# Optimization experiments

Measured on AMD Instinct MI355X. Metric: run time of the kernel, lower is better.

## Reference

```python
import jax, jax.numpy as jnp
import numpy as np

B, C, T = 8, 512, 2048
INTER = C // 2            # inter_channels default = in_channels // 2
L = 2                     # temporal_layer_num


def _pos_encoding(c, t):
    # standard sinusoidal PE, returned as (c, t) to match pos().permute(0,2,1)
    pos = jnp.arange(t, dtype=jnp.float32)[:, None]            # (t,1)
    i = jnp.arange(0, c, 2, dtype=jnp.float32)                 # (c/2,)
    div = jnp.exp(-(jnp.log(10000.0) / c) * i)                 # (c/2,)
    pe = jnp.zeros((t, c), dtype=jnp.float32)
    pe = pe.at[:, 0::2].set(jnp.sin(pos * div))
    pe = pe.at[:, 1::2].set(jnp.cos(pos * div))
    return pe.T                                                # (c,t)


def _conv1x1(w, b, x):
    # kernel_size=1 Conv1d == channel GEMM: w (o,c), x (b,c,t) -> (b,o,t)
    return jnp.einsum('oc,bct->bot', w, x) + b[:, None]


def _temporal_conv(x, w, d):
    # Conv2d(1, c, kernel=(3, c), dilation=(d,1), padding=(d,0), no bias)
    # x (b,c,t) -> input (b,1,t,c); kernel w (c,3,c) -> (c,1,3,c); out (b,c,t,1)
    x4 = x.transpose(0, 2, 1)[:, None, :, :]
    k = w[:, None, :, :]
    y = jax.lax.conv_general_dilated(
        x4, k, window_strides=(1, 1), padding=((d, d), (0, 0)),
        rhs_dilation=(d, 1), dimension_numbers=('NCHW', 'OIHW', 'NCHW'))
    return y[..., 0]                                           # (b,c,t)


def setup_inputs() -> dict:
    key = jax.random.key(0)
    ks = jax.random.split(key, 12)
    n = lambda k, shape, s=0.02: jax.random.normal(k, shape, jnp.float32) * s
    return {
        'x': jax.random.normal(ks[0], (B, C, T), jnp.float32),
        'w_tr': n(ks[1], (C, C)),
        'b_tr': jnp.zeros((C,), jnp.float32),
        'w_tc': n(ks[2], (L, C, 3, C), 0.001),   # init.normal_(std=0.001)
        'w_g': n(ks[3], (L + 1, INTER, C)),
        'b_g': jnp.zeros((L + 1, INTER), jnp.float32),
        'w_th': n(ks[4], (L + 1, INTER, C)),
        'b_th': jnp.zeros((L + 1, INTER), jnp.float32),
        'w_ph': n(ks[5], (L + 1, INTER, C)),
        'b_ph': jnp.zeros((L + 1, INTER), jnp.float32),
        'w_W': n(ks[6], (C, INTER * (L + 1))),
        'b_W': jnp.zeros((C,), jnp.float32),
        'gamma': 1.0 + n(ks[7], (C,)),
        'beta': n(ks[8], (C,)),
    }


def reference(x, w_tr, b_tr, w_tc, w_g, b_g, w_th, b_th, w_ph, b_ph,
              w_W, b_W, gamma, beta):
    b, c, t = x.shape
    x = x + _pos_encoding(c, t)[None]                 # add positional encoding
    x = jax.nn.relu(_conv1x1(w_tr, b_tr, x))          # tranpos_w + relu

    # temporal dilated-conv features, then raw x as last branch
    temps = [_temporal_conv(x, w_tc[i], i + 1) for i in range(w_tc.shape[0])]
    temps.append(x)

    ys = []
    for i, tx in enumerate(temps):
        gx = _conv1x1(w_g[i], b_g[i], tx)             # (b,inter,t)
        th = _conv1x1(w_th[i], b_th[i], tx)           # (b,inter,t)
        ph = _conv1x1(w_ph[i], b_ph[i], tx)           # (b,inter,t)
        f = jax.nn.softmax(jnp.einsum('bit,bis->bts', th, ph), axis=-1)
        ys.append(jnp.einsum('bts,bis->bit', f, gx))  # (b,inter,t)

    y = jnp.concatenate(ys, axis=1)                   # (b, 3*inter, t)
    wy = _conv1x1(w_W, b_W, y)                        # (b,c,t)
    # BatchNorm1d, training-mode batch stats over (batch, time)
    mean = wy.mean(axis=(0, 2), keepdims=True)
    var = wy.var(axis=(0, 2), keepdims=True)
    wy = (wy - mean) * jax.lax.rsqrt(var + 1e-5)
    wy = wy * gamma[None, :, None] + beta[None, :, None]
    return wy + x
```

## Files before the change

kernel.cpp:

```cpp
#include <hip/hip_runtime.h>

#define B_ 8
#define C_ 512
#define T_ 2048
#define I_ 256
#define TP_ (T_ + 4)

typedef _Float16 f16x8 __attribute__((ext_vector_type(8)));
typedef float f32x4 __attribute__((ext_vector_type(4)));
typedef unsigned short u16;
typedef unsigned short u16x4 __attribute__((ext_vector_type(4)));

__device__ __forceinline__ u16 f2h(float f) {
    _Float16 h = (_Float16)f;
    return *(u16*)&h;
}
__device__ __forceinline__ float h2f(u16 u) {
    _Float16 h = *(_Float16*)&u;
    return (float)h;
}

#define AS1 __attribute__((address_space(1)))
#define AS3 __attribute__((address_space(3)))
__device__ __forceinline__ void gload16(const u16* g, u16* l) {
    __builtin_amdgcn_global_load_lds((const AS1 void*)(const void*)g,
                                     (AS3 void*)(void*)l, 16, 0, 0);
}

template <int WMODE, bool BIAS, bool RELU, bool TCONV>
__global__ __launch_bounds__(256) void mfma_gemm(
    const u16* __restrict__ A, long aB, int aZdiv, int lda,
    const u16* __restrict__ Bm, long bB, int ldb, int bZmod,
    const float* __restrict__ bias, int biasStride,
    float* __restrict__ Cf, u16* __restrict__ Cn, long cB, int ldc,
    u16* __restrict__ Ct, long ctB, int ldct, int ctOff,
    int K, int dShift)
{
    __shared__ u16 sA[128 * 64];
    __shared__ u16 sB[128 * 64];
    const int z = blockIdx.z;
    const int zw = z / aZdiv;
    const int zb = z % bZmod;
    const int m0 = blockIdx.y * 128, n0 = blockIdx.x * 128;
    const int tid = threadIdx.x;
    const int lane = tid & 63, wv = tid >> 6;
    const int wm = wv >> 1, wn = wv & 1;
    const int l15 = lane & 15, l4 = lane >> 4;

    const u16* Ab = A + (long)zw * aB + (long)m0 * lda;
    const u16* Bb = Bm + (long)zb * bB + (long)n0 * ldb;

    const int srow = wv * 32 + (lane >> 3);
    const int sk16 = (lane & 7) ^ (lane >> 3);

    f32x4 acc[4][4];
    #pragma unroll
    for (int i = 0; i < 4; ++i)
        #pragma unroll
        for (int j = 0; j < 4; ++j) acc[i][j] = (f32x4){0.f, 0.f, 0.f, 0.f};

    for (int k0 = 0; k0 < K; k0 += 64) {
        int bCol = k0;
        int rOff = 0;
        if (TCONV) {
            const int kh = k0 >> 9;
            const int d = dShift ? dShift : 1 + (z >> 3);
            rOff = (kh - 1) * d;
            bCol = k0 & 511;
        }
        #pragma unroll
        for (int ch = 0; ch < 4; ++ch) {
            gload16(Ab + (long)(srow + ch * 8) * lda + k0 + sk16 * 8,
                    &sA[wv * 2048 + ch * 512]);
            gload16(Bb + (long)(srow + ch * 8 + rOff) * ldb + bCol + sk16 * 8,
                    &sB[wv * 2048 + ch * 512]);
        }
        __syncthreads();
        #pragma unroll
        for (int kk = 0; kk < 2; ++kk) {
            f16x8 af[4], bfr[4];
            #pragma unroll
            for (int f = 0; f < 4; ++f) {
                const int ra = wm * 64 + f * 16 + l15;
                af[f] = *(const f16x8*)&sA[ra * 64 + ((((kk << 2) | l4) ^ (ra & 7)) << 3)];
                const int rb = wn * 64 + f * 16 + l15;
                bfr[f] = *(const f16x8*)&sB[rb * 64 + ((((kk << 2) | l4) ^ (rb & 7)) << 3)];
            }
            #pragma unroll
            for (int mi = 0; mi < 4; ++mi)
                #pragma unroll
                for (int ni = 0; ni < 4; ++ni)
                    acc[mi][ni] = __builtin_amdgcn_mfma_f32_16x16x32_f16(
                        af[mi], bfr[ni], acc[mi][ni], 0, 0, 0);
        }
        __syncthreads();
    }

    #pragma unroll
    for (int mi = 0; mi < 4; ++mi) {
        const int mb = m0 + wm * 64 + mi * 16 + l4 * 4;
        float bv[4] = {0.f, 0.f, 0.f, 0.f};
        if (BIAS) {
            const float* bp = bias + (long)zw * biasStride;
            #pragma unroll
            for (int r = 0; r < 4; ++r) bv[r] = bp[mb + r];
        }
        #pragma unroll
        for (int ni = 0; ni < 4; ++ni) {
            const int nb = n0 + wn * 64 + ni * 16 + l15;
            float v[4];
            #pragma unroll
            for (int r = 0; r < 4; ++r) {
                v[r] = acc[mi][ni][r] + bv[r];
                if (RELU) v[r] = fmaxf(v[r], 0.f);
            }
            if (WMODE & 1) {
                #pragma unroll
                for (int r = 0; r < 4; ++r)
                    Cf[(long)z * cB + (long)(mb + r) * ldc + nb] = v[r];
            }
            if (WMODE & 2) {
                #pragma unroll
                for (int r = 0; r < 4; ++r)
                    Cn[(long)z * cB + (long)(mb + r) * ldc + nb] = f2h(v[r]);
            }
            if (WMODE & 4) {
                u16x4 pk;
                #pragma unroll
                for (int r = 0; r < 4; ++r) pk[r] = f2h(v[r]);
                *(u16x4*)&Ct[(long)z * ctB + (long)nb * ldct + ctOff + mb] = pk;
            }
        }
    }
}

__global__ __launch_bounds__(512) void flash_attn(
    const u16* __restrict__ thA, const u16* __restrict__ phA,
    const u16* __restrict__ gxA, u16* __restrict__ oH,
    float* __restrict__ mH, float* __restrict__ lH)
{
    __shared__ u16 sK[64 * 256];
    __shared__ u16 sV[256 * 64];
    __shared__ u16 sP[8 * 16 * 64];

    const int flat = (blockIdx.z * 24 + blockIdx.y) * 16 + blockIdx.x;
    const int swz = (flat & 7) * 96 + (flat >> 3);
    const int u = swz % 384;
    const int qb = u & 15, z = u >> 4;
    const int half = swz / 384;
    const int t0 = qb * 128;
    const int sBase = half * (T_ / 2);
    const int tid = threadIdx.x;
    const int lane = tid & 63, wv = tid >> 6;
    const int l15 = lane & 15, l4 = lane >> 4;

    const u16* Qz = thA + (long)z * (T_ * I_);
    const u16* Kz = phA + (long)z * (T_ * I_);
    const u16* Vz = gxA + (long)z * ((long)I_ * T_);

    f16x8 qf[8];
    {
        const u16* qrow = Qz + (long)(t0 + wv * 16 + l15) * I_ + l4 * 8;
        #pragma unroll
        for (int ks = 0; ks < 8; ++ks) qf[ks] = *(const f16x8*)(qrow + ks * 32);
    }

    f32x4 oacc[16];
    #pragma unroll
    for (int i = 0; i < 16; ++i) oacc[i] = (f32x4){0.f, 0.f, 0.f, 0.f};
    float mrun[4] = {-1e30f, -1e30f, -1e30f, -1e30f};
    float lrun[4] = {0.f, 0.f, 0.f, 0.f};

    const int krow = tid >> 5;
    const int kk16 = (tid & 31) ^ (krow & 7);
    const int vrow = tid >> 3;
    const int vk16 = (tid & 7) ^ (vrow & 7);

    for (int s0 = sBase; s0 < sBase + T_ / 2; s0 += 64) {
        #pragma unroll
        for (int is = 0; is < 4; ++is) {
            gload16(Kz + (long)(s0 + is * 16 + krow) * I_ + kk16 * 8,
                    &sK[is * 4096 + tid * 8]);
            gload16(Vz + (long)(is * 64 + vrow) * T_ + s0 + vk16 * 8,
                    &sV[is * 4096 + tid * 8]);
        }
        __syncthreads();

        f32x4 sacc[4];
        #pragma unroll
        for (int nf = 0; nf < 4; ++nf) sacc[nf] = (f32x4){0.f, 0.f, 0.f, 0.f};
        #pragma unroll
        for (int nf = 0; nf < 4; ++nf) {
            const int srow = nf * 16 + l15;
            #pragma unroll
            for (int ks = 0; ks < 8; ++ks) {
                f16x8 kf = *(const f16x8*)&sK[srow * 256 + ((((ks << 2) | l4) ^ (srow & 7)) << 3)];
                sacc[nf] = __builtin_amdgcn_mfma_f32_16x16x32_f16(qf[ks], kf, sacc[nf], 0, 0, 0);
            }
        }

        float scale[4];
        #pragma unroll
        for (int r = 0; r < 4; ++r) {
            float v0 = fmaxf(fmaxf(sacc[0][r], sacc[1][r]),
                             fmaxf(sacc[2][r], sacc[3][r]));
            #pragma unroll
            for (int o = 8; o; o >>= 1) v0 = fmaxf(v0, __shfl_xor(v0, o, 64));
            const float mnew = fmaxf(mrun[r], v0);
            scale[r] = __expf(mrun[r] - mnew);
            mrun[r] = mnew;
        }
        float rsum[4] = {0.f, 0.f, 0.f, 0.f};
        #pragma unroll
        for (int nf = 0; nf < 4; ++nf) {
            #pragma unroll
            for (int r = 0; r < 4; ++r) {
                const float p = __expf(sacc[nf][r] - mrun[r]);
                rsum[r] += p;
                const int tl = l4 * 4 + r;
                const int sl = l15 + nf * 16;
                sP[wv * 1024 + tl * 64 + ((((sl >> 3) ^ (tl & 7)) << 3) | (sl & 7))] = f2h(p);
            }
        }
        #pragma unroll
        for (int r = 0; r < 4; ++r) {
            #pragma unroll
            for (int o = 8; o; o >>= 1) rsum[r] += __shfl_xor(rsum[r], o, 64);
            lrun[r] = lrun[r] * scale[r] + rsum[r];
        }
        #pragma unroll
        for (int nf = 0; nf < 16; ++nf)
            #pragma unroll
            for (int r = 0; r < 4; ++r) oacc[nf][r] *= scale[r];

        f16x8 pa[2];
        #pragma unroll
        for (int kk = 0; kk < 2; ++kk)
            pa[kk] = *(const f16x8*)&sP[wv * 1024 + l15 * 64 + ((((kk << 2) | l4) ^ (l15 & 7)) << 3)];
        #pragma unroll
        for (int nf = 0; nf < 16; ++nf) {
            const int dvr = nf * 16 + l15;
            #pragma unroll
            for (int kk = 0; kk < 2; ++kk) {
                f16x8 vf = *(const f16x8*)&sV[dvr * 64 + ((((kk << 2) | l4) ^ (dvr & 7)) << 3)];
                oacc[nf] = __builtin_amdgcn_mfma_f32_16x16x32_f16(pa[kk], vf, oacc[nf], 0, 0, 0);
            }
        }
        __syncthreads();
    }

    #pragma unroll
    for (int r = 0; r < 4; ++r) {
        const int t = t0 + wv * 16 + l4 * 4 + r;
        const long row = ((long)half * 24 + z) * T_ + t;
        u16* dst = oH + row * I_ + l15;
        #pragma unroll
        for (int nf = 0; nf < 16; ++nf)
            dst[nf * 16] = f2h(oacc[nf][r]);
        if (l15 == 0) { mH[row] = mrun[r]; lH[row] = lrun[r]; }
    }
}

__global__ __launch_bounds__(256) void combine_kernel(
    const u16* __restrict__ oH, const float* __restrict__ mH,
    const float* __restrict__ lH, u16* __restrict__ YT)
{
    const long idx = (long)blockIdx.x * 256 + threadIdx.x;
    const int z = (int)(idx / (T_ * (I_ / 8)));
    const long rem = idx % (T_ * (I_ / 8));
    const int t = (int)(rem / (I_ / 8));
    const int dv0 = (int)(rem % (I_ / 8)) * 8;
    const long row0 = (long)z * T_ + t;
    const long row1 = ((long)24 + z) * T_ + t;
    const float m0 = mH[row0], m1 = mH[row1];
    const float l0 = lH[row0], l1 = lH[row1];
    const float m = fmaxf(m0, m1);
    const float a0 = __expf(m0 - m), a1 = __expf(m1 - m);
    const float inv = 1.f / (l0 * a0 + l1 * a1);
    const uint4 p0 = *(const uint4*)&oH[row0 * I_ + dv0];
    const uint4 p1 = *(const uint4*)&oH[row1 * I_ + dv0];
    const u16* b0 = (const u16*)&p0;
    const u16* b1 = (const u16*)&p1;
    uint4 ov;
    u16* bo = (u16*)&ov;
    #pragma unroll
    for (int j = 0; j < 8; ++j)
        bo[j] = f2h((h2f(b0[j]) * a0 + h2f(b1[j]) * a1) * inv);
    const int br = z >> 3, b = z & 7;
    *(uint4*)&YT[((long)b * T_ + t) * (3 * I_) + br * I_ + dv0] = ov;
}

__global__ __launch_bounds__(256) void to_f16(
    const float* __restrict__ s, u16* __restrict__ d, long n4)
{
    const long i = (long)blockIdx.x * 256 + threadIdx.x;
    if (i >= n4) return;
    const float4 v = ((const float4*)s)[i];
    u16x4 pk = {f2h(v.x), f2h(v.y), f2h(v.z), f2h(v.w)};
    ((u16x4*)d)[i] = pk;
}

__global__ __launch_bounds__(256) void peT_kernel(float* __restrict__ peT)
{
    const int idx = blockIdx.x * 256 + threadIdx.x;
    const int c = idx & (C_ - 1), t = idx >> 9;
    const float i2 = (float)(c & ~1);
    const float freq = expf(-(9.210340371976184f / (float)C_) * i2);
    const float ang = (float)t * freq;
    peT[idx] = (c & 1) ? cosf(ang) : sinf(ang);
}

__global__ __launch_bounds__(256) void xpose_add(
    const float* __restrict__ x, const float* __restrict__ peT,
    u16* __restrict__ xpeT)
{
    __shared__ float tile[64][65];
    const int b = blockIdx.z;
    const int t0 = blockIdx.x * 64, c0 = blockIdx.y * 64;
    const int rr = threadIdx.x >> 4, cc4 = (threadIdx.x & 15) << 2;
    #pragma unroll
    for (int p = 0; p < 4; ++p) {
        const int row = rr + p * 16;
        const float4 v = *(const float4*)&x[((long)b * C_ + c0 + row) * T_ + t0 + cc4];
        tile[row][cc4 + 0] = v.x; tile[row][cc4 + 1] = v.y;
        tile[row][cc4 + 2] = v.z; tile[row][cc4 + 3] = v.w;
    }
    __syncthreads();
    #pragma unroll
    for (int p = 0; p < 4; ++p) {
        const int tt = rr + p * 16;
        const int gt = t0 + tt;
        const float4 pv = *(const float4*)&peT[(long)gt * C_ + c0 + cc4];
        u16x4 pk = {f2h(tile[cc4 + 0][tt] + pv.x),
                    f2h(tile[cc4 + 1][tt] + pv.y),
                    f2h(tile[cc4 + 2][tt] + pv.z),
                    f2h(tile[cc4 + 3][tt] + pv.w)};
        *(u16x4*)&xpeT[((long)b * T_ + gt) * C_ + c0 + cc4] = pk;
    }
}

__global__ __launch_bounds__(256) void stats_kernel(
    const float* __restrict__ wy, float* __restrict__ mean,
    float* __restrict__ rstd)
{
    __shared__ float sm[8];
    const int o = blockIdx.x, tid = threadIdx.x;
    float s = 0.f, ss = 0.f;
    for (int idx = tid; idx < B_ * T_; idx += 256) {
        const int b = idx >> 11, t = idx & (T_ - 1);
        const float vv = wy[((long)b * C_ + o) * T_ + t];
        s += vv; ss += vv * vv;
    }
    #pragma unroll
    for (int off = 32; off; off >>= 1) {
        s += __shfl_xor(s, off, 64);
        ss += __shfl_xor(ss, off, 64);
    }
    if ((tid & 63) == 0) { sm[tid >> 6] = s; sm[4 + (tid >> 6)] = ss; }
    __syncthreads();
    if (tid == 0) {
        s = sm[0] + sm[1] + sm[2] + sm[3];
        ss = sm[4] + sm[5] + sm[6] + sm[7];
        const float mu = s / (float)(B_ * T_);
        const float var = ss / (float)(B_ * T_) - mu * mu;
        mean[o] = mu;
        rstd[o] = rsqrtf(var + 1e-5f);
    }
}

__global__ __launch_bounds__(256) void final_kernel(
    float* __restrict__ out, const u16* __restrict__ x1n,
    const float* __restrict__ mean, const float* __restrict__ rstd,
    const float* __restrict__ gamma, const float* __restrict__ beta)
{
    const long i4 = (long)blockIdx.x * 256 + threadIdx.x;
    const long i = i4 * 4;
    const int c = (int)((i / T_) & (C_ - 1));
    const float4 w = ((const float4*)out)[i4];
    const uint2 xv = ((const uint2*)x1n)[i4];
    const u16* xb = (const u16*)&xv;
    const float mu = mean[c];
    const float a = rstd[c] * gamma[c];
    const float bb = beta[c];
    float4 r;
    r.x = (w.x - mu) * a + bb + h2f(xb[0]);
    r.y = (w.y - mu) * a + bb + h2f(xb[1]);
    r.z = (w.z - mu) * a + bb + h2f(xb[2]);
    r.w = (w.w - mu) * a + bb + h2f(xb[3]);
    ((float4*)out)[i4] = r;
}

extern "C" void kernel_launch(void* const* d_in, const int* in_sizes, int n_in,
                              void* d_out, int out_size, void* d_ws, size_t ws_size,
                              hipStream_t stream)
{
    const float* x    = (const float*)d_in[0];
    const float* w_tr = (const float*)d_in[1];
    const float* b_tr = (const float*)d_in[2];
    const float* w_tc = (const float*)d_in[3];
    const float* w_g  = (const float*)d_in[4];
    const float* b_g  = (const float*)d_in[5];
    const float* w_th = (const float*)d_in[6];
    const float* b_th = (const float*)d_in[7];
    const float* w_ph = (const float*)d_in[8];
    const float* b_ph = (const float*)d_in[9];
    const float* w_W  = (const float*)d_in[10];
    const float* b_W  = (const float*)d_in[11];
    const float* gamma = (const float*)d_in[12];
    const float* beta  = (const float*)d_in[13];
    float* out = (float*)d_out;

    char* pp = (char*)d_ws;
    auto nextp = [&](long bytes) { char* r = pp; pp += (bytes + 255) & ~255L; return r; };
    const long TC  = (long)T_ * C_;
    const long CT  = (long)C_ * T_;
    const long TPC = (long)TP_ * C_;
    const long TI  = (long)T_ * I_;
    const long IT  = (long)I_ * T_;

    float* peT  = (float*)nextp(4L * T_ * C_);
    u16* xpeT   = (u16*)nextp(2L * B_ * TC);
    u16* x1n    = (u16*)nextp(2L * B_ * CT);
    u16* txAll  = (u16*)nextp(2L * 3 * B_ * TPC);
    u16* gxAll  = (u16*)nextp(2L * 3 * B_ * IT);
    u16* thAll  = (u16*)nextp(2L * 3 * B_ * TI);
    u16* phAll  = (u16*)nextp(2L * 3 * B_ * TI);
    u16* YT     = (u16*)nextp(2L * B_ * T_ * 3 * I_);
    u16* oH     = (u16*)nextp(2L * 2 * 24 * T_ * I_);
    float* mH   = (float*)nextp(4L * 2 * 24 * T_);
    float* lH   = (float*)nextp(4L * 2 * 24 * T_);
    u16* w_trb  = (u16*)nextp(2L * C_ * C_);
    u16* w_tcb  = (u16*)nextp(2L * 2 * C_ * 3 * C_);
    u16* w_gb   = (u16*)nextp(2L * 3 * I_ * C_);
    u16* w_thph = (u16*)nextp(2L * 6 * I_ * C_);
    u16* w_Wb   = (u16*)nextp(2L * C_ * 3 * I_);
    float* biasAll = (float*)nextp(4L * 6 * I_);
    float* meanb = (float*)nextp(4L * C_);
    float* rstdb = (float*)nextp(4L * C_);

    u16* slab0 = txAll;
    u16* slab2 = txAll + 2L * B_ * TPC;

    auto cvt = [&](const float* s, u16* d, long n) {
        to_f16<<<(int)((n / 4 + 255) / 256), 256, 0, stream>>>(s, d, n / 4);
    };
    cvt(w_tr, w_trb, (long)C_ * C_);
    cvt(w_tc, w_tcb, 2L * C_ * 3 * C_);
    cvt(w_g,  w_gb,  3L * I_ * C_);
    cvt(w_th, w_thph, 3L * I_ * C_);
    cvt(w_ph, w_thph + 3L * I_ * C_, 3L * I_ * C_);
    cvt(w_W,  w_Wb,  (long)C_ * 3 * I_);
    hipMemcpyAsync(biasAll, b_th, 3L * I_ * 4, hipMemcpyDeviceToDevice, stream);
    hipMemcpyAsync(biasAll + 3 * I_, b_ph, 3L * I_ * 4, hipMemcpyDeviceToDevice, stream);

    peT_kernel<<<(T_ * C_) / 256, 256, 0, stream>>>(peT);
    xpose_add<<<dim3(T_ / 64, C_ / 64, B_), 256, 0, stream>>>(x, peT, xpeT);

    hipMemsetAsync(slab2, 0, 2L * B_ * TPC, stream);

    mfma_gemm<6, true, true, false><<<dim3(16, 4, 8), 256, 0, stream>>>(
        w_trb, 0, 1, C_, xpeT, TC, C_, 9999, b_tr, 0,
        nullptr, x1n, CT, T_, slab2 + 2 * C_, TPC, C_, 0, C_, 0);

    mfma_gemm<4, false, false, true><<<dim3(16, 4, 16), 256, 0, stream>>>(
        w_tcb, (long)C_ * 3 * C_, 8, 3 * C_, slab2 + 2 * C_, TPC, C_, 8, nullptr, 0,
        nullptr, nullptr, 0, 0, slab0 + 2 * C_, TPC, C_, 0, 3 * C_, 0);

    mfma_gemm<2, true, false, false><<<dim3(16, 2, 24), 256, 0, stream>>>(
        w_gb, (long)I_ * C_, 8, C_, txAll + 2 * C_, TPC, C_, 9999, b_g, I_,
        nullptr, gxAll, IT, T_, nullptr, 0, 0, 0, C_, 0);

    mfma_gemm<4, true, false, false><<<dim3(16, 2, 48), 256, 0, stream>>>(
        w_thph, (long)I_ * C_, 8, C_, txAll + 2 * C_, TPC, C_, 24, biasAll, I_,
        nullptr, nullptr, 0, 0, thAll, TI, I_, 0, C_, 0);

    flash_attn<<<dim3(16, 24, 2), 512, 0, stream>>>(thAll, phAll, gxAll, oH, mH, lH);
    combine_kernel<<<(int)(24L * T_ * (I_ / 8) / 256), 256, 0, stream>>>(oH, mH, lH, YT);

    mfma_gemm<1, true, false, false><<<dim3(16, 4, 8), 256, 0, stream>>>(
        w_Wb, 0, 1, 3 * I_, YT, (long)T_ * 3 * I_, 3 * I_, 9999, b_W, 0,
        out, nullptr, CT, T_, nullptr, 0, 0, 0, 3 * I_, 0);

    stats_kernel<<<C_, 256, 0, stream>>>(out, meanb, rstdb);
    final_kernel<<<(int)(B_ * C_ * T_ / 4 / 256), 256, 0, stream>>>(
        out, x1n, meanb, rstdb, gamma, beta);
}
```

Measured before the change: 474.7 us.

## Double-buffer K/V tiles in flash attention with 32-wide key blocks

```diff
diff --git a/kernel.cpp b/kernel.cpp
--- a/kernel.cpp
+++ b/kernel.cpp
@@ -139,9 +139,9 @@
     const u16* __restrict__ gxA, u16* __restrict__ oH,
     float* __restrict__ mH, float* __restrict__ lH)
 {
-    __shared__ u16 sK[64 * 256];
-    __shared__ u16 sV[256 * 64];
-    __shared__ u16 sP[8 * 16 * 64];
+    __shared__ u16 sK[2][32 * 256];
+    __shared__ u16 sV[2][256 * 32];
+    __shared__ u16 sP[8 * 16 * 32];
 
     const int flat = (blockIdx.z * 24 + blockIdx.y) * 16 + blockIdx.x;
     const int swz = (flat & 7) * 96 + (flat >> 3);
@@ -171,30 +171,35 @@
     float mrun[4] = {-1e30f, -1e30f, -1e30f, -1e30f};
     float lrun[4] = {0.f, 0.f, 0.f, 0.f};
 
-    const int krow = tid >> 5;
-    const int kk16 = (tid & 31) ^ (krow & 7);
-    const int vrow = tid >> 3;
-    const int vk16 = (tid & 7) ^ (vrow & 7);
-
-    for (int s0 = sBase; s0 < sBase + T_ / 2; s0 += 64) {
-        #pragma unroll
-        for (int is = 0; is < 4; ++is) {
-            gload16(Kz + (long)(s0 + is * 16 + krow) * I_ + kk16 * 8,
-                    &sK[is * 4096 + tid * 8]);
-            gload16(Vz + (long)(is * 64 + vrow) * T_ + s0 + vk16 * 8,
-                    &sV[is * 4096 + tid * 8]);
-        }
-        __syncthreads();
-
-        f32x4 sacc[4];
-        #pragma unroll
-        for (int nf = 0; nf < 4; ++nf) sacc[nf] = (f32x4){0.f, 0.f, 0.f, 0.f};
-        #pragma unroll
-        for (int nf = 0; nf < 4; ++nf) {
+    auto stage = [&](int buf, int s0) {
+        #pragma unroll
+        for (int rr = 0; rr < 2; ++rr) {
+            const int fk = rr * 512 + tid;
+            const int ksr = fk >> 5, kslot = fk & 31;
+            gload16(Kz + (long)(s0 + ksr) * I_ + ((kslot ^ (ksr & 7)) << 3),
+                    &sK[buf][fk * 8]);
+            const int dv = fk >> 2, vs = fk & 3;
+            gload16(Vz + (long)dv * T_ + s0 + ((vs ^ (dv & 3)) << 3),
+                    &sV[buf][fk * 8]);
+        }
+    };
+
+    stage(0, sBase);
+    __syncthreads();
+
+    int cur = 0;
+    for (int s0 = sBase; s0 < sBase + T_ / 2; s0 += 32) {
+        if (s0 + 32 < sBase + T_ / 2) stage(cur ^ 1, s0 + 32);
+
+        f32x4 sacc[2];
+        #pragma unroll
+        for (int nf = 0; nf < 2; ++nf) sacc[nf] = (f32x4){0.f, 0.f, 0.f, 0.f};
+        #pragma unroll
+        for (int nf = 0; nf < 2; ++nf) {
             const int srow = nf * 16 + l15;
             #pragma unroll
             for (int ks = 0; ks < 8; ++ks) {
-                f16x8 kf = *(const f16x8*)&sK[srow * 256 + ((((ks << 2) | l4) ^ (srow & 7)) << 3)];
+                f16x8 kf = *(const f16x8*)&sK[cur][srow * 256 + ((((ks << 2) | l4) ^ (srow & 7)) << 3)];
                 sacc[nf] = __builtin_amdgcn_mfma_f32_16x16x32_f16(qf[ks], kf, sacc[nf], 0, 0, 0);
             }
         }
@@ -202,8 +207,7 @@
         float scale[4];
         #pragma unroll
         for (int r = 0; r < 4; ++r) {
-            float v0 = fmaxf(fmaxf(sacc[0][r], sacc[1][r]),
-                             fmaxf(sacc[2][r], sacc[3][r]));
+            float v0 = fmaxf(sacc[0][r], sacc[1][r]);
             #pragma unroll
             for (int o = 8; o; o >>= 1) v0 = fmaxf(v0, __shfl_xor(v0, o, 64));
             const float mnew = fmaxf(mrun[r], v0);
@@ -212,14 +216,14 @@
         }
         float rsum[4] = {0.f, 0.f, 0.f, 0.f};
         #pragma unroll
-        for (int nf = 0; nf < 4; ++nf) {
+        for (int nf = 0; nf < 2; ++nf) {
             #pragma unroll
             for (int r = 0; r < 4; ++r) {
                 const float p = __expf(sacc[nf][r] - mrun[r]);
                 rsum[r] += p;
                 const int tl = l4 * 4 + r;
                 const int sl = l15 + nf * 16;
-                sP[wv * 1024 + tl * 64 + ((((sl >> 3) ^ (tl & 7)) << 3) | (sl & 7))] = f2h(p);
+                sP[wv * 512 + tl * 32 + ((((sl >> 3) ^ (tl & 3)) << 3) | (sl & 7))] = f2h(p);
             }
         }
         #pragma unroll
@@ -233,20 +237,15 @@
             #pragma unroll
             for (int r = 0; r < 4; ++r) oacc[nf][r] *= scale[r];
 
-        f16x8 pa[2];
-        #pragma unroll
-        for (int kk = 0; kk < 2; ++kk)
-            pa[kk] = *(const f16x8*)&sP[wv * 1024 + l15 * 64 + ((((kk << 2) | l4) ^ (l15 & 7)) << 3)];
+        f16x8 pa = *(const f16x8*)&sP[wv * 512 + l15 * 32 + ((l4 ^ (l15 & 3)) << 3)];
         #pragma unroll
         for (int nf = 0; nf < 16; ++nf) {
             const int dvr = nf * 16 + l15;
-            #pragma unroll
-            for (int kk = 0; kk < 2; ++kk) {
-                f16x8 vf = *(const f16x8*)&sV[dvr * 64 + ((((kk << 2) | l4) ^ (dvr & 7)) << 3)];
-                oacc[nf] = __builtin_amdgcn_mfma_f32_16x16x32_f16(pa[kk], vf, oacc[nf], 0, 0, 0);
-            }
+            f16x8 vf = *(const f16x8*)&sV[cur][dvr * 32 + ((l4 ^ (dvr & 3)) << 3)];
+            oacc[nf] = __builtin_amdgcn_mfma_f32_16x16x32_f16(pa, vf, oacc[nf], 0, 0, 0);
         }
         __syncthreads();
+        cur ^= 1;
     }
 
     #pragma unroll
```

Result: slower. 564.0 us (+18.8%).
